# Performance work log

Hardware: AMD Instinct MI355X
Metric: run time of the kernel (lower is better)

## Reference

```python
import jax, jax.numpy as jnp
import numpy as np

N = 100000

def _gcn_layer(x, W, b, row, col, n):
    # x: [N, Fin] -> lin -> [N, Fout]
    h = x @ W + b
    # degree over row (includes self loops), dtype follows x
    deg = jnp.zeros((n,), dtype=h.dtype).at[row].add(jnp.ones_like(row, dtype=h.dtype))
    dis = deg ** -0.5
    norm = dis[row] * dis[col]                      # [E]
    msg = norm[:, None] * h[row]                    # gather + scale: [E, Fout]
    return jax.ops.segment_sum(msg, col, num_segments=n)  # scatter-add at targets


def setup_inputs() -> dict:
    key = jax.random.key(0)
    ks = jax.random.split(key, 10)
    x = jax.random.normal(ks[0], (N, 32), dtype=jnp.float32)
    feat = jax.random.normal(ks[1], (N, 32), dtype=jnp.float32)
    edge_index = jax.random.randint(ks[2], (2, 1600000), 0, N, dtype=jnp.int64)
    # params (torch Linear stored as [in, out] here; y = x @ W + b)
    def lin(k, fin, fout):
        s = 1.0 / np.sqrt(fin)
        kw, kb = jax.random.split(k)
        W = jax.random.uniform(kw, (fin, fout), minval=-s, maxval=s, dtype=jnp.float32)
        b = jax.random.uniform(kb, (fout,), minval=-s, maxval=s, dtype=jnp.float32)
        return W, b
    W1, b1 = lin(ks[3], 64, 64)
    W2, b2 = lin(ks[4], 64, 64)
    Wfc, bfc = lin(ks[5], 64, 64)
    return {"x": x, "feat": feat, "edge_index": edge_index,
            "W1": W1, "b1": b1, "W2": W2, "b2": b2, "Wfc": Wfc, "bfc": bfc}


def reference(x, feat, edge_index, W1, b1, W2, b2, Wfc, bfc):
    n = x.shape[0]
    h = jnp.concatenate([x, feat], axis=-1)          # [N, 64]
    # add self loops once (same augmented edge set used by every layer)
    loops = jnp.arange(n, dtype=edge_index.dtype)
    row = jnp.concatenate([edge_index[0], loops])
    col = jnp.concatenate([edge_index[1], loops])
    h = jax.nn.relu(_gcn_layer(h, W1, b1, row, col, n))
    h = jax.nn.relu(_gcn_layer(h, W2, b2, row, col, n))
    return jax.nn.relu(h @ Wfc + bfc)                # [N, 64]
```

## Files before the change

kernel.cpp:

```cpp
#include <hip/hip_runtime.h>
#include <hip/hip_bf16.h>


#define FDIM 64
#define NPART 4
#define GPB 64
#define NB 256
#define BW 512
#define MAXP 1024
#define GPLIN 1024

typedef __hip_bfloat16 bf16;
typedef short v8s __attribute__((ext_vector_type(8)));
typedef float v4f __attribute__((ext_vector_type(4)));

static __device__ __forceinline__ float ulo2f(unsigned u) {
    union { unsigned x; float f; } v; v.x = u << 16; return v.f;
}
static __device__ __forceinline__ float uhi2f(unsigned u) {
    union { unsigned x; float f; } v; v.x = u & 0xFFFF0000u; return v.f;
}
static __device__ __forceinline__ unsigned f2bu(float f) {
    bf16 b = __float2bfloat16(f);
    return (unsigned)(*(unsigned short*)&b);
}

__global__ __launch_bounds__(1024)
void k_h2(const int* __restrict__ row, const int* __restrict__ col,
          unsigned* __restrict__ part, int* __restrict__ M,
          int E, int n, int psize, int psize4, int P, int CH) {
    __shared__ unsigned sm[6256];
    int t = threadIdx.x, b = blockIdx.x;
    if (b < NPART * GPB) {
        int p = b >> 6, g = b & 63;
        int base = p * psize;
        int lim = n - base; if (lim > psize) lim = psize;
        int lim4 = (lim + 3) >> 2;
        for (int i = t; i < lim4; i += 1024) sm[i] = 0u;
        __syncthreads();
        for (int e = (g * 1024 + t) * 4; e < E; e += GPB * 4096) {
            int4 r4 = *(const int4*)&row[e];
            int r0 = r4.x - base, r1 = r4.y - base, r2 = r4.z - base, r3 = r4.w - base;
            if ((unsigned)r0 < (unsigned)lim) atomicAdd(&sm[r0 >> 2], 1u << ((r0 & 3) * 8));
            if ((unsigned)r1 < (unsigned)lim) atomicAdd(&sm[r1 >> 2], 1u << ((r1 & 3) * 8));
            if ((unsigned)r2 < (unsigned)lim) atomicAdd(&sm[r2 >> 2], 1u << ((r2 & 3) * 8));
            if ((unsigned)r3 < (unsigned)lim) atomicAdd(&sm[r3 >> 2], 1u << ((r3 & 3) * 8));
        }
        __syncthreads();
        unsigned* dst = part + ((size_t)p * GPB + g) * psize4;
        for (int i = t; i < lim4; i += 1024) dst[i] = sm[i];
    } else {
        int cb = b - NPART * GPB;
        int* h = (int*)sm;
        for (int i = t; i < P; i += 1024) h[i] = 0;
        __syncthreads();
        int s = cb * CH, e = min(s + CH, E);
        for (int i = s + t * 4; i < e; i += 4096) {
            int4 c4 = *(const int4*)&col[i];
            atomicAdd(&h[c4.x >> 9], 1);
            atomicAdd(&h[c4.y >> 9], 1);
            atomicAdd(&h[c4.z >> 9], 1);
            atomicAdd(&h[c4.w >> 9], 1);
        }
        __syncthreads();
        for (int p = t; p < P; p += 1024) M[p * NB + cb] = h[p];
    }
}

__global__ void k_ds1(const unsigned* __restrict__ part, float* __restrict__ dis,
                      int* __restrict__ M, int* __restrict__ bsum,
                      int n, int psize4, int ndis4, int P) {
    __shared__ int sc[256];
    int t = threadIdx.x, b = blockIdx.x;
    if (b < ndis4) {
        int i4 = b * 256 + t;
        int i = i4 * 4;
        if (i >= n) return;
        int p = i4 / psize4, loc = i4 - p * psize4;
        const unsigned* src = part + (size_t)p * GPB * psize4 + loc;
        unsigned s0 = 0, s1 = 0, s2 = 0, s3 = 0;
        #pragma unroll 8
        for (int g = 0; g < GPB; ++g) {
            unsigned u = src[(size_t)g * psize4];
            s0 += u & 255u; s1 += (u >> 8) & 255u;
            s2 += (u >> 16) & 255u; s3 += u >> 24;
        }
        dis[i] = rsqrtf((float)s0 + 1.0f);
        if (i + 1 < n) dis[i + 1] = rsqrtf((float)s1 + 1.0f);
        if (i + 2 < n) dis[i + 2] = rsqrtf((float)s2 + 1.0f);
        if (i + 3 < n) dis[i + 3] = rsqrtf((float)s3 + 1.0f);
    } else {
        int sb = b - ndis4;
        int i = sb * 256 + t;
        int v = M[i];
        sc[t] = v;
        __syncthreads();
        for (int d = 1; d < 256; d <<= 1) {
            int u = (t >= d) ? sc[t - d] : 0;
            __syncthreads(); sc[t] += u; __syncthreads();
        }
        M[i] = sc[t] - v;
        if (t == 255) bsum[sb] = sc[255];
    }
}

__global__ __launch_bounds__(1024)
void k_csc(const int* __restrict__ row, const int* __restrict__ col,
           const int* __restrict__ M, const int* __restrict__ bsum,
           int* __restrict__ s4, int E, int CH, int P) {
    __shared__ int sc[256];
    __shared__ int bs[256];
    __shared__ int cur[MAXP];
    int t = threadIdx.x, b = blockIdx.x;
    if (t < 256) { int v = (t < P) ? bsum[t] : 0; sc[t] = v; bs[t] = v; }
    __syncthreads();
    for (int d = 1; d < 256; d <<= 1) {
        int u = (t < 256 && t >= d) ? sc[t - d] : 0;
        __syncthreads();
        if (t < 256) sc[t] += u;
        __syncthreads();
    }
    if (t < 256) bs[t] = sc[t] - bs[t];
    __syncthreads();
    for (int p = t; p < P; p += 1024) cur[p] = bs[p] + M[p * NB + b];
    __syncthreads();
    int s = b * CH, e = min(s + CH, E);
    for (int i = s + t * 4; i < e; i += 4096) {
        int4 r4 = *(const int4*)&row[i];
        int4 c4 = *(const int4*)&col[i];
        int p0 = atomicAdd(&cur[c4.x >> 9], 1);
        s4[p0] = (r4.x << 9) | (c4.x & 511);
        int p1 = atomicAdd(&cur[c4.y >> 9], 1);
        s4[p1] = (r4.y << 9) | (c4.y & 511);
        int p2 = atomicAdd(&cur[c4.z >> 9], 1);
        s4[p2] = (r4.z << 9) | (c4.z & 511);
        int p3 = atomicAdd(&cur[c4.w >> 9], 1);
        s4[p3] = (r4.w << 9) | (c4.w & 511);
    }
}

__global__ __launch_bounds__(1024)
void k_fsort(const int* __restrict__ s4, const int* __restrict__ bsum,
             int* __restrict__ rows4, int* __restrict__ off,
             int n, int E, int P) {
    __shared__ int sc[256];
    __shared__ int bs[256];
    __shared__ int hist[BW];
    __shared__ int loff[BW];
    __shared__ int tmp[256];
    int t = threadIdx.x, b = blockIdx.x;
    if (t < 256) { int v = (t < P) ? bsum[t] : 0; sc[t] = v; bs[t] = v; }
    __syncthreads();
    for (int d = 1; d < 256; d <<= 1) {
        int u = (t < 256 && t >= d) ? sc[t - d] : 0;
        __syncthreads();
        if (t < 256) sc[t] += u;
        __syncthreads();
    }
    if (t < 256) bs[t] = sc[t] - bs[t];
    __syncthreads();
    int gs = bs[b];
    int ge = gs + bsum[b];
    int c0 = b << 9;
    int lim = n - c0; if (lim > BW) lim = BW;
    for (int i = t; i < BW; i += 1024) hist[i] = 0;
    __syncthreads();
    for (int i = gs + t; i < ge; i += 1024)
        atomicAdd(&hist[s4[i] & 511], 1);
    __syncthreads();
    int s0 = 0, s1v = 0, ps = 0;
    if (t < 256) {
        s0 = hist[2 * t]; s1v = hist[2 * t + 1];
        ps = s0 + s1v;
        tmp[t] = ps;
    }
    __syncthreads();
    for (int d = 1; d < 256; d <<= 1) {
        int u = (t < 256 && t >= d) ? tmp[t - d] : 0;
        __syncthreads();
        if (t < 256) tmp[t] += u;
        __syncthreads();
    }
    if (t < 256) {
        int ex = tmp[t] - ps;
        loff[2 * t] = ex;
        loff[2 * t + 1] = ex + s0;
    }
    __syncthreads();
    for (int i = t; i < lim; i += 1024) off[c0 + i] = gs + loff[i];
    if (b == P - 1 && t == 0) off[n] = E;
    __syncthreads();
    for (int i = gs + t; i < ge; i += 1024) {
        int v2 = s4[i];
        int pos = gs + atomicAdd(&loff[v2 & 511], 1);
        rows4[pos] = v2 >> 9;
    }
}

__global__ __launch_bounds__(256, 4)
void k_linc(const float* __restrict__ x, const float* __restrict__ feat,
            const float* __restrict__ W, const float* __restrict__ bvec,
            const float* __restrict__ dis, bf16* __restrict__ g1, int n) {
    __shared__ float sIn[4][FDIM];
    int t = threadIdx.x;
    int local = t >> 6, j = t & 63;
    float Wreg[FDIM];
    #pragma unroll
    for (int k = 0; k < FDIM; ++k) Wreg[k] = W[k * FDIM + j];
    float bj = bvec[j];
    int gw = blockIdx.x * 4 + local;
    int nwl = GPLIN * 4;
    for (int w = gw; w < n; w += nwl) {
        sIn[local][j] = (j < 32) ? x[(size_t)w * 32 + j]
                                 : feat[(size_t)w * 32 + (j - 32)];
        __threadfence_block();
        float o = bj;
        #pragma unroll
        for (int k4 = 0; k4 < 16; ++k4) {
            float4 h4 = *(const float4*)&sIn[local][k4 * 4];
            o = fmaf(h4.x, Wreg[4 * k4 + 0], o);
            o = fmaf(h4.y, Wreg[4 * k4 + 1], o);
            o = fmaf(h4.z, Wreg[4 * k4 + 2], o);
            o = fmaf(h4.w, Wreg[4 * k4 + 3], o);
        }
        g1[(size_t)w * FDIM + j] = __float2bfloat16(dis[w] * o);
        __threadfence_block();
    }
}

__global__ __launch_bounds__(256, 8)
void k_gather(const int* __restrict__ rows4, const int* __restrict__ off,
              const float* __restrict__ dis, const bf16* __restrict__ g,
              bf16* __restrict__ a, int n) {
    int t = blockIdx.x * blockDim.x + threadIdx.x;
    int w = t >> 6;
    if (w >= n) return;
    int lane = threadIdx.x & 63;
    int h = lane >> 5;
    int j2 = lane & 31;
    const unsigned* g32 = (const unsigned*)g;
    float acc0 = 0.0f, acc1 = 0.0f;
    int s = off[w], e = off[w + 1];
    int k = s;
    for (; k + 16 <= e; k += 16) {
        #pragma unroll
        for (int i = 0; i < 8; ++i) {
            int r = rows4[k + 2 * i + h];
            unsigned u = g32[(size_t)r * 32 + j2];
            acc0 += ulo2f(u);
            acc1 += uhi2f(u);
        }
    }
    if (k < e) {
        #pragma unroll
        for (int i = 0; i < 8; ++i) {
            int idx = k + 2 * i + h;
            int r = rows4[min(idx, e - 1)];
            unsigned u = g32[(size_t)r * 32 + j2];
            float wg = (idx < e) ? 1.0f : 0.0f;
            acc0 = fmaf(wg, ulo2f(u), acc0);
            acc1 = fmaf(wg, uhi2f(u), acc1);
        }
    }
    acc0 += __shfl_xor(acc0, 32, 64);
    acc1 += __shfl_xor(acc1, 32, 64);
    if (h == 0) {
        unsigned su = g32[(size_t)w * 32 + j2];
        float dv = dis[w];
        float v0 = fmaxf(dv * (acc0 + ulo2f(su)), 0.0f);
        float v1 = fmaxf(dv * (acc1 + uhi2f(su)), 0.0f);
        ((unsigned*)a)[(size_t)w * 32 + j2] = f2bu(v0) | (f2bu(v1) << 16);
    }
}

template <bool FINAL>
__global__ __launch_bounds__(256, 4)
void k_mat(const bf16* __restrict__ A, const float* __restrict__ W,
           const float* __restrict__ bvec, const float* __restrict__ dis,
           void* __restrict__ outp, int n) {
    __shared__ __align__(16) bf16 sWt[FDIM * FDIM];
    int t = threadIdx.x;
    for (int idx = t; idx < FDIM * FDIM; idx += 256) {
        int kk = idx >> 6, nn = idx & 63;
        sWt[nn * FDIM + kk] = __float2bfloat16(W[idx]);
    }
    __syncthreads();
    int wave = t >> 6, lane = t & 63;
    int quad = lane >> 4, l15 = lane & 15;
    v8s bfr[4][2];
    #pragma unroll
    for (int nt = 0; nt < 4; ++nt) {
        #pragma unroll
        for (int kf = 0; kf < 2; ++kf)
            bfr[nt][kf] = *(const v8s*)&sWt[(nt * 16 + l15) * FDIM + kf * 32 + quad * 8];
    }
    float bj[4];
    #pragma unroll
    for (int nt = 0; nt < 4; ++nt) bj[nt] = bvec[nt * 16 + l15];

    int ntiles = (n + 15) >> 4;
    int step = gridDim.x * 4;
    for (int tile = blockIdx.x * 4 + wave; tile < ntiles; tile += step) {
        int m0 = tile << 4;
        int mA = m0 + l15; if (mA >= n) mA = n - 1;
        v8s af0 = *(const v8s*)&A[(size_t)mA * FDIM + quad * 8];
        v8s af1 = *(const v8s*)&A[(size_t)mA * FDIM + 32 + quad * 8];
        v4f acc[4];
        #pragma unroll
        for (int nt = 0; nt < 4; ++nt) {
            acc[nt] = (v4f){0.f, 0.f, 0.f, 0.f};
            acc[nt] = __builtin_amdgcn_mfma_f32_16x16x32_bf16(af0, bfr[nt][0], acc[nt], 0, 0, 0);
            acc[nt] = __builtin_amdgcn_mfma_f32_16x16x32_bf16(af1, bfr[nt][1], acc[nt], 0, 0, 0);
        }
        #pragma unroll
        for (int r = 0; r < 4; ++r) {
            int node = m0 + quad * 4 + r;
            if (node >= n) continue;
            float dv = FINAL ? 0.0f : dis[node];
            #pragma unroll
            for (int nt = 0; nt < 4; ++nt) {
                int j = nt * 16 + l15;
                float o = acc[nt][r] + bj[nt];
                if (FINAL) ((float*)outp)[(size_t)node * FDIM + j] = fmaxf(o, 0.0f);
                else ((bf16*)outp)[(size_t)node * FDIM + j] = __float2bfloat16(dv * o);
            }
        }
    }
}

extern "C" void kernel_launch(void* const* d_in, const int* in_sizes, int n_in,
                              void* d_out, int out_size, void* d_ws, size_t ws_size,
                              hipStream_t stream) {
    const float* x    = (const float*)d_in[0];
    const float* feat = (const float*)d_in[1];
    const int*   ei   = (const int*)d_in[2];
    const float* W1   = (const float*)d_in[3];
    const float* b1   = (const float*)d_in[4];
    const float* W2   = (const float*)d_in[5];
    const float* b2   = (const float*)d_in[6];
    const float* Wfc  = (const float*)d_in[7];
    const float* bfc  = (const float*)d_in[8];
    float* out = (float*)d_out;

    const int n = in_sizes[0] / 32;
    const int E = in_sizes[2] / 2;
    const int* row = ei;
    const int* col = ei + E;

    const int psize = (((n + NPART - 1) / NPART) + 3) & ~3;
    const int psize4 = psize >> 2;
    const int P  = (n + BW - 1) / BW;
    const int CH = (((E + NB - 1) / NB) + 3) & ~3;
    const int total = P * NB;
    const int ndis4 = (((n + 3) / 4) + 255) / 256;

    int*   off  = (int*)d_ws;
    float* dis  = (float*)(off + (size_t)n + 1);
    int*   M    = (int*)(dis + n);
    int*   bsum = M + (size_t)total;
    int*   s4    = bsum + 256;
    int*   rows4 = s4 + E;
    size_t co = (size_t)(rows4 + E - (int*)d_ws);
    co = (co + 3) & ~(size_t)3;
    bf16*  bufA  = (bf16*)((int*)d_ws + co);
    bf16*  bufB  = bufA + (size_t)n * FDIM;
    unsigned* part = (unsigned*)bufA;

    k_h2<<<NPART * GPB + NB, 1024, 0, stream>>>(row, col, part, M, E, n,
                                                psize, psize4, P, CH);
    k_ds1<<<ndis4 + P, 256, 0, stream>>>(part, dis, M, bsum, n, psize4, ndis4, P);
    k_csc<<<NB, 1024, 0, stream>>>(row, col, M, bsum, s4, E, CH, P);
    k_fsort<<<P, 1024, 0, stream>>>(s4, bsum, rows4, off, n, E, P);
    k_linc<<<GPLIN, 256, 0, stream>>>(x, feat, W1, b1, dis, bufA, n);
    k_gather<<<(n + 3) / 4, 256, 0, stream>>>(rows4, off, dis, bufA, bufB, n);
    k_mat<false><<<512, 256, 0, stream>>>(bufB, W2, b2, dis, bufA, n);
    k_gather<<<(n + 3) / 4, 256, 0, stream>>>(rows4, off, dis, bufA, bufB, n);
    k_mat<true><<<512, 256, 0, stream>>>(bufB, Wfc, bfc, dis, out, n);
}
```

Baseline: 272.0 us.

## Split feature matrix into 16-column slabs and gather per slab in passes

The intermediate bf16 feature buffers move from row-major [N,64] to four column slabs of [N,16], written by the linear and matmul kernels and read slab-wise by the MFMA loads. The gather kernel now launches four passes, one per slab, with each wave handling 8 edges per iteration over 8 lanes of features. Each pass touches a 3.2MB slab that can stay resident in cache, replacing random gathers over the full 12.8MB table. In exchange, the row index list is read four times, each gather moves only 32 bytes, and the kernel adds a three-step shuffle reduction. Nontemporal loads and stores are also used for the indices and outputs.

```diff
diff --git a/kernel.cpp b/kernel.cpp
--- a/kernel.cpp
+++ b/kernel.cpp
@@ -208,6 +208,7 @@
     #pragma unroll
     for (int k = 0; k < FDIM; ++k) Wreg[k] = W[k * FDIM + j];
     float bj = bvec[j];
+    int slab = j >> 4, jo = j & 15;
     int gw = blockIdx.x * 4 + local;
     int nwl = GPLIN * 4;
     for (int w = gw; w < n; w += nwl) {
@@ -223,7 +224,8 @@
             o = fmaf(h4.z, Wreg[4 * k4 + 2], o);
             o = fmaf(h4.w, Wreg[4 * k4 + 3], o);
         }
-        g1[(size_t)w * FDIM + j] = __float2bfloat16(dis[w] * o);
+        g1[(size_t)slab * n * 16 + (size_t)w * 16 + jo] =
+            __float2bfloat16(dis[w] * o);
         __threadfence_block();
     }
 }
@@ -231,45 +233,46 @@
 __global__ __launch_bounds__(256, 8)
 void k_gather(const int* __restrict__ rows4, const int* __restrict__ off,
               const float* __restrict__ dis, const bf16* __restrict__ g,
-              bf16* __restrict__ a, int n) {
-    int t = blockIdx.x * blockDim.x + threadIdx.x;
-    int w = t >> 6;
+              bf16* __restrict__ a, int n, int nbp) {
+    int b = blockIdx.x;
+    int pass = b / nbp;
+    int bb = b - pass * nbp;
+    int w = bb * 4 + (threadIdx.x >> 6);
     if (w >= n) return;
     int lane = threadIdx.x & 63;
-    int h = lane >> 5;
-    int j2 = lane & 31;
-    const unsigned* g32 = (const unsigned*)g;
+    int es = lane >> 3;
+    int j2 = lane & 7;
+    const unsigned* gs = (const unsigned*)g + (size_t)pass * n * 8;
+    unsigned* as = (unsigned*)a + (size_t)pass * n * 8;
     float acc0 = 0.0f, acc1 = 0.0f;
     int s = off[w], e = off[w + 1];
     int k = s;
-    for (; k + 16 <= e; k += 16) {
-        #pragma unroll
-        for (int i = 0; i < 8; ++i) {
-            int r = rows4[k + 2 * i + h];
-            unsigned u = g32[(size_t)r * 32 + j2];
-            acc0 += ulo2f(u);
-            acc1 += uhi2f(u);
-        }
+    for (; k + 8 <= e; k += 8) {
+        int r = __builtin_nontemporal_load(rows4 + k + es);
+        unsigned u = gs[(size_t)r * 8 + j2];
+        acc0 += ulo2f(u);
+        acc1 += uhi2f(u);
     }
     if (k < e) {
-        #pragma unroll
-        for (int i = 0; i < 8; ++i) {
-            int idx = k + 2 * i + h;
-            int r = rows4[min(idx, e - 1)];
-            unsigned u = g32[(size_t)r * 32 + j2];
-            float wg = (idx < e) ? 1.0f : 0.0f;
-            acc0 = fmaf(wg, ulo2f(u), acc0);
-            acc1 = fmaf(wg, uhi2f(u), acc1);
-        }
-    }
-    acc0 += __shfl_xor(acc0, 32, 64);
-    acc1 += __shfl_xor(acc1, 32, 64);
-    if (h == 0) {
-        unsigned su = g32[(size_t)w * 32 + j2];
+        int idx = k + es;
+        int r = __builtin_nontemporal_load(rows4 + min(idx, e - 1));
+        unsigned u = gs[(size_t)r * 8 + j2];
+        float wg = (idx < e) ? 1.0f : 0.0f;
+        acc0 = fmaf(wg, ulo2f(u), acc0);
+        acc1 = fmaf(wg, uhi2f(u), acc1);
+    }
+    #pragma unroll
+    for (int m = 8; m <= 32; m <<= 1) {
+        acc0 += __shfl_xor(acc0, m, 64);
+        acc1 += __shfl_xor(acc1, m, 64);
+    }
+    if (es == 0) {
+        unsigned su = gs[(size_t)w * 8 + j2];
         float dv = dis[w];
         float v0 = fmaxf(dv * (acc0 + ulo2f(su)), 0.0f);
         float v1 = fmaxf(dv * (acc1 + uhi2f(su)), 0.0f);
-        ((unsigned*)a)[(size_t)w * 32 + j2] = f2bu(v0) | (f2bu(v1) << 16);
+        __builtin_nontemporal_store(f2bu(v0) | (f2bu(v1) << 16),
+                                    as + (size_t)w * 8 + j2);
     }
 }
 
@@ -298,13 +301,17 @@
     #pragma unroll
     for (int nt = 0; nt < 4; ++nt) bj[nt] = bvec[nt * 16 + l15];
 
+    const bf16* A0 = A + (size_t)(quad >> 1) * n * 16;
+    const bf16* A1 = A + (size_t)(2 + (quad >> 1)) * n * 16;
+    int ho = (quad & 1) * 8;
+
     int ntiles = (n + 15) >> 4;
     int step = gridDim.x * 4;
     for (int tile = blockIdx.x * 4 + wave; tile < ntiles; tile += step) {
         int m0 = tile << 4;
         int mA = m0 + l15; if (mA >= n) mA = n - 1;
-        v8s af0 = *(const v8s*)&A[(size_t)mA * FDIM + quad * 8];
-        v8s af1 = *(const v8s*)&A[(size_t)mA * FDIM + 32 + quad * 8];
+        v8s af0 = *(const v8s*)&A0[(size_t)mA * 16 + ho];
+        v8s af1 = *(const v8s*)&A1[(size_t)mA * 16 + ho];
         v4f acc[4];
         #pragma unroll
         for (int nt = 0; nt < 4; ++nt) {
@@ -321,8 +328,12 @@
             for (int nt = 0; nt < 4; ++nt) {
                 int j = nt * 16 + l15;
                 float o = acc[nt][r] + bj[nt];
-                if (FINAL) ((float*)outp)[(size_t)node * FDIM + j] = fmaxf(o, 0.0f);
-                else ((bf16*)outp)[(size_t)node * FDIM + j] = __float2bfloat16(dv * o);
+                if (FINAL) {
+                    ((float*)outp)[(size_t)node * FDIM + j] = fmaxf(o, 0.0f);
+                } else {
+                    ((bf16*)outp)[(size_t)nt * n * 16 + (size_t)node * 16 + l15] =
+                        __float2bfloat16(dv * o);
+                }
             }
         }
     }
@@ -353,6 +364,7 @@
     const int CH = (((E + NB - 1) / NB) + 3) & ~3;
     const int total = P * NB;
     const int ndis4 = (((n + 3) / 4) + 255) / 256;
+    const int nbp = (n + 3) / 4;
 
     int*   off  = (int*)d_ws;
     float* dis  = (float*)(off + (size_t)n + 1);
@@ -372,8 +384,8 @@
     k_csc<<<NB, 1024, 0, stream>>>(row, col, M, bsum, s4, E, CH, P);
     k_fsort<<<P, 1024, 0, stream>>>(s4, bsum, rows4, off, n, E, P);
     k_linc<<<GPLIN, 256, 0, stream>>>(x, feat, W1, b1, dis, bufA, n);
-    k_gather<<<(n + 3) / 4, 256, 0, stream>>>(rows4, off, dis, bufA, bufB, n);
+    k_gather<<<4 * nbp, 256, 0, stream>>>(rows4, off, dis, bufA, bufB, n, nbp);
     k_mat<false><<<512, 256, 0, stream>>>(bufB, W2, b2, dis, bufA, n);
-    k_gather<<<(n + 3) / 4, 256, 0, stream>>>(rows4, off, dis, bufA, bufB, n);
+    k_gather<<<4 * nbp, 256, 0, stream>>>(rows4, off, dis, bufA, bufB, n, nbp);
     k_mat<true><<<512, 256, 0, stream>>>(bufB, Wfc, bfc, dis, out, n);
 }
```

Measured after the change: 498.9 us. +83.5%, slower.
